# Kernel tuning notes

Measured on AMD Instinct MI355X. Metric: run time of the kernel, lower is better.

The kernel has to match this reference:

```python
import jax, jax.numpy as jnp
import numpy as np

H, DK, DV = 4, 64, 64        # heads, key/value head dims (hidden=256)
M, TOPK = 4, 2               # num memories, router top-k
GN, EPS, COND_SCALE = 16.0, 1e-5, 1.0


def setup_inputs() -> dict:
    key = jax.random.key(0)
    ks = jax.random.split(key, 12)
    B, Q, K, D = 8, 64, 256, 256
    w = lambda k, shape, fan: jax.random.normal(k, shape, jnp.float32) / np.sqrt(fan).astype(np.float32)
    return {
        "query": jax.random.normal(ks[0], (B, Q, D), jnp.float32),
        "keyval": jax.random.normal(ks[1], (B, K, D), jnp.float32),
        "attention_mask_kv": jnp.ones((B, K), jnp.int32),
        "W_cond": w(ks[2], (D, D), D),
        "W_q": w(ks[3], (D, H * DK), D),
        "W_k": w(ks[4], (D, H * DK), D),
        "W_v": w(ks[5], (D, H * DV), D),
        "W_gk1": w(ks[6], (D, 16), D),
        "W_gk2": w(ks[7], (16, H * DK), 16),
        "b_gk2": jnp.zeros((H * DK,), jnp.float32),
        "W_router": w(ks[8], (D, M), D),
        "norm_w": jnp.ones((DV,), jnp.float32),
        "W_o": w(ks[9], (H * DV, D), H * DV),
    }


def _mem_last(q_last, k, v, gk, sel, wgt):
    """Last-token output of one gated linear-attention memory.
    S_t = diag(exp(gk_t)) S_{t-1} + k_t v_t^T ; o_T = q_T S_T.
    q_last: (N,H,DK); k,gk: (N,K,H,DK); v: (N,K,H,DV); sel,wgt: (N,K)."""
    k_e = k * sel[:, :, None, None]
    v_e = v * wgt[:, :, None, None]
    gk_e = gk * sel[:, :, None, None]          # unselected tokens: no decay, no update
    G = jnp.cumsum(gk_e, axis=1)               # (N,K,H,DK), log decays
    decay = jnp.exp(G[:, -1:, :, :] - G)       # remaining decay to last step, <= 1
    s = jnp.einsum('nhd,nthd->nth', q_last, k_e * decay)
    return jnp.einsum('nth,nthv->nhv', s, v_e)


def reference(query, keyval, attention_mask_kv, W_cond, W_q, W_k, W_v,
              W_gk1, W_gk2, b_gk2, W_router, norm_w, W_o):
    B, Q, D = query.shape
    K = keyval.shape[1]
    N = B * Q
    # broadcast KV expansion + cond injection
    cond = (query @ W_cond) * COND_SCALE                         # (B,Q,D)
    x = (keyval[:, None, :, :] + cond[:, :, None, :]).reshape(N, K, D)
    m = jnp.broadcast_to(attention_mask_kv[:, None, :].astype(x.dtype), (B, Q, K)).reshape(N, K)
    # projections
    q = (x @ W_q).reshape(N, K, H, DK)
    k = (x @ W_k).reshape(N, K, H, DK) * m[:, :, None, None]
    v = (x @ W_v).reshape(N, K, H, DV) * m[:, :, None, None]
    gk = (jax.nn.log_sigmoid(x @ W_gk1 @ W_gk2 + b_gk2) / GN).reshape(N, K, H, DK)
    gk = gk * m[:, :, None, None]
    # router: softmax -> top-k -> renormalize
    router_logits = (x @ W_router).reshape(N * K, M)
    probs = jax.nn.softmax(router_logits, axis=-1)
    topv, topi = jax.lax.top_k(probs, TOPK)
    topv = topv / jnp.sum(topv, axis=-1, keepdims=True)
    w_mem = jnp.sum(jax.nn.one_hot(topi, M, dtype=x.dtype) * topv[..., None], axis=-2)
    w_mem = w_mem.reshape(N, K, M)
    # shared memory (always on) + routed memories
    q_last = q[:, -1]
    ones = jnp.ones((N, K), x.dtype)
    o = _mem_last(q_last, k, v, gk, ones, ones)
    for e in range(M):
        we = w_mem[:, :, e]
        o = o + _mem_last(q_last, k, v, gk, (we > 0).astype(x.dtype), we)
    # per-head RMSNorm + output projection
    o = o * jax.lax.rsqrt(jnp.mean(o * o, axis=-1, keepdims=True) + EPS) * norm_w
    out = (o.reshape(N, H * DV) @ W_o).reshape(B, Q, D)
    return out, router_logits
```

## Files before the change

### kernel.cpp

```cpp
#include <hip/hip_runtime.h>
#include <math.h>

#define Hh   4
#define Bb   8
#define Qq   64
#define Kk   256
#define Dd   256
#define Nn   (Bb * Qq)
#define GNf  16.0f
#define EPSf 1e-5f

#define SKV  776
#define SCB  1032

struct GemmS { float As[16][136]; float Ws[16][136]; };
struct RtrS  { float WrT[4][260]; };
union  WorkS { GemmS g; RtrS r; };

__device__ __forceinline__ float wred(float x) {
#pragma unroll
    for (int off = 32; off > 0; off >>= 1)
        x += __shfl_xor(x, off, 64);
    return x;
}

__device__ void gemm64(GemmS& g, const float* __restrict__ A, int lda, int Mv,
                       const float* __restrict__ B, int bn,
                       float* __restrict__ C, int ldc)
{
    float (*As)[68] = (float(*)[68])(&g.As[0][0]);
    const int tid = threadIdx.x;
    const int ty = tid >> 4, tx = tid & 15;
    const int am = tid >> 2, ak = (tid & 3) << 2;
    const int wk = tid >> 4, wc = (tid & 15) << 3;
    const int ams = (am < Mv) ? am : (Mv - 1);

    float acc[4][8] = {};
    const float* aptr = A + (size_t)ams * lda + ak;
    const float* bptr = B + wk * 256 + bn + wc;
    float4 av = *(const float4*)aptr;
    float4 b0 = *(const float4*)bptr;
    float4 b1 = *(const float4*)(bptr + 4);

    for (int k0 = 0; k0 < 256; k0 += 16) {
        __syncthreads();
        As[ak + 0][am] = av.x; As[ak + 1][am] = av.y;
        As[ak + 2][am] = av.z; As[ak + 3][am] = av.w;
        *(float4*)&g.Ws[wk][wc]     = b0;
        *(float4*)&g.Ws[wk][wc + 4] = b1;
        __syncthreads();
        if (k0 + 16 < 256) {
            av = *(const float4*)(aptr + k0 + 16);
            b0 = *(const float4*)(bptr + (k0 + 16) * 256);
            b1 = *(const float4*)(bptr + (k0 + 16) * 256 + 4);
        }
#pragma unroll
        for (int kk = 0; kk < 16; ++kk) {
            const float4 a4 = *(const float4*)&As[kk][ty << 2];
            const float4 w0 = *(const float4*)&g.Ws[kk][tx << 2];
            const float4 w1 = *(const float4*)&g.Ws[kk][64 + (tx << 2)];
            const float a_[4] = {a4.x, a4.y, a4.z, a4.w};
            const float w_[8] = {w0.x, w0.y, w0.z, w0.w, w1.x, w1.y, w1.z, w1.w};
#pragma unroll
            for (int i = 0; i < 4; ++i)
#pragma unroll
                for (int jj = 0; jj < 8; ++jj)
                    acc[i][jj] = fmaf(a_[i], w_[jj], acc[i][jj]);
        }
    }

#pragma unroll
    for (int i = 0; i < 4; ++i) {
        const int rr = (ty << 2) + i;
        if (rr < Mv) {
            *(float4*)(C + (size_t)rr * ldc + (tx << 2)) =
                make_float4(acc[i][0], acc[i][1], acc[i][2], acc[i][3]);
            *(float4*)(C + (size_t)rr * ldc + 64 + (tx << 2)) =
                make_float4(acc[i][4], acc[i][5], acc[i][6], acc[i][7]);
        }
    }
}

__device__ void router_region(RtrS& rs, const float* __restrict__ A,
                              const float* __restrict__ Wr,
                              float* __restrict__ C, int ldc, int row0)
{
    const int tid = threadIdx.x;
    for (int idx = tid; idx < 1024; idx += 256)
        rs.WrT[idx & 3][idx >> 2] = Wr[idx];
    __syncthreads();
    const int row = row0 + (tid >> 2), c = tid & 3;
    const float* a = A + (size_t)row * 256;
    float acc = 0.f;
#pragma unroll 8
    for (int k4 = 0; k4 < 64; ++k4) {
        const float4 avv = *(const float4*)(a + (k4 << 2));
        const float4 wvv = *(const float4*)&rs.WrT[c][k4 << 2];
        acc = fmaf(avv.x, wvv.x, acc);
        acc = fmaf(avv.y, wvv.y, acc);
        acc = fmaf(avv.z, wvv.z, acc);
        acc = fmaf(avv.w, wvv.w, acc);
    }
    C[(size_t)row * ldc + c] = acc;
}

__device__ void wg_region(const float* __restrict__ Wg1,
                          const float* __restrict__ Wg2,
                          float* __restrict__ Wg, int k0)
{
    const int c = threadIdx.x;
    float w2[16];
#pragma unroll
    for (int i = 0; i < 16; ++i) w2[i] = Wg2[i * 256 + c];
#pragma unroll
    for (int r = 0; r < 16; ++r) {
        const int k = k0 + r;
        float s = 0.f;
#pragma unroll
        for (int i = 0; i < 16; ++i) s = fmaf(Wg1[k * 16 + i], w2[i], s);
        Wg[k * 256 + c] = s;
    }
}

__global__ __launch_bounds__(256) void k1(
    const float* __restrict__ query, const float* __restrict__ keyval,
    const float* __restrict__ W_cond, const float* __restrict__ W_q,
    const float* __restrict__ W_gk1, const float* __restrict__ W_gk2,
    const float* __restrict__ W_router,
    float* __restrict__ Wg, float* __restrict__ cond,
    float* __restrict__ qlast, float* __restrict__ KVb)
{
    __shared__ WorkS S;
    const int id = blockIdx.x;
    if (id < 16) {
        wg_region(W_gk1, W_gk2, Wg, id * 16);
    } else if (id < 32) {
        const int t = id - 16;
        gemm64(S.g, query + (size_t)(t >> 1) * 64 * 256, 256, 64,
               W_cond, (t & 1) * 128,
               cond + (size_t)(t >> 1) * 64 * 256 + (t & 1) * 128, 256);
    } else if (id < 34) {
        gemm64(S.g, keyval + 255 * 256, Kk * Dd, 8, W_q, (id - 32) * 128,
               qlast + (id - 32) * 128, 256);
    } else {
        router_region(S.r, keyval, W_router, KVb + 768, SKV, (id - 34) * 64);
    }
}

__global__ __launch_bounds__(256) void k2(
    const float* __restrict__ keyval, const float* __restrict__ cond,
    const float* __restrict__ W_q, const float* __restrict__ W_k,
    const float* __restrict__ W_v, const float* __restrict__ Wg,
    const float* __restrict__ W_router,
    float* __restrict__ KVb, float* __restrict__ Cb)
{
    __shared__ WorkS S;
    const int id = blockIdx.x;
    if (id < 192) {
        const int rt = id / 6, ct = id % 6;
        const float* Bsel = (ct < 2) ? W_k : (ct < 4) ? W_v : Wg;
        gemm64(S.g, keyval + (size_t)rt * 64 * 256, 256, 64,
               Bsel, (ct & 1) * 128,
               KVb + (size_t)rt * 64 * SKV + (ct >> 1) * 256 + (ct & 1) * 128,
               SKV);
    } else if (id < 256) {
        const int t = id - 192, rg = t >> 4, rt = (t & 15) >> 1, ct = t & 1;
        const float* Bsel = (rg == 0) ? W_q : (rg == 1) ? W_k
                          : (rg == 2) ? W_v : Wg;
        gemm64(S.g, cond + (size_t)rt * 64 * 256, 256, 64,
               Bsel, ct * 128,
               Cb + (size_t)rt * 64 * SCB + rg * 256 + ct * 128, SCB);
    } else {
        router_region(S.r, cond, W_router, Cb + 1024, SCB, (id - 256) * 64);
    }
}

__global__ __launch_bounds__(256) void mom_fused(
    const float* __restrict__ KVb, const float* __restrict__ Cb,
    const float* __restrict__ qlast, const float* __restrict__ b_gk2,
    const int* __restrict__ mask, const float* __restrict__ W_o,
    const float* __restrict__ norm_w, float* __restrict__ out,
    float* __restrict__ logits)
{
    __shared__ float4 wm[Kk];
    __shared__ float  Pt[4][16][68];
    __shared__ float  sbuf[4][16];
    __shared__ float  onorm[Dd];

    const int n = blockIdx.x;
    const int b = n >> 6;
    const int j = threadIdx.x;
    const int lane = j & 63;
    const int wv = j >> 6;

    const float qc = Cb[(size_t)n * SCB + j];
    const float kc = Cb[(size_t)n * SCB + 256 + j];
    const float vc = Cb[(size_t)n * SCB + 512 + j];
    const float pc = Cb[(size_t)n * SCB + 768 + j] + b_gk2[j];
    const float4 rc = *(const float4*)(Cb + (size_t)n * SCB + 1024);

    const int* pm = mask + b * Kk;

    {
        const float4 kvr = *(const float4*)(KVb + (size_t)(b * Kk + j) * SKV + 768);
        float l[4] = {kvr.x + rc.x, kvr.y + rc.y, kvr.z + rc.z, kvr.w + rc.w};
        *(float4*)(logits + ((size_t)n * Kk + j) * 4) =
            make_float4(l[0], l[1], l[2], l[3]);

        int i1 = 0;
#pragma unroll
        for (int q = 1; q < 4; ++q) if (l[q] > l[i1]) i1 = q;
        int i2 = -1;
#pragma unroll
        for (int q = 0; q < 4; ++q) {
            if (q == i1) continue;
            if (i2 < 0 || l[q] > l[i2]) i2 = q;
        }
        const float mx = fmaxf(l[i1], l[i2]);
        const float e1 = __expf(l[i1] - mx);
        const float e2 = __expf(l[i2] - mx);
        const float inv = 1.f / (e1 + e2);
        float w[4] = {0.f, 0.f, 0.f, 0.f};
        w[i1] = e1 * inv;
        w[i2] = e2 * inv;
        wm[j] = make_float4(w[0], w[1], w[2], w[3]);
    }
    __syncthreads();

    const float ql  = qlast[b * 256 + j] + qc;
    const float qkc = ql * kc;
    const float* pkv = KVb + (size_t)b * Kk * SKV + j;

    float E0 = 1.f, E1 = 1.f, E2 = 1.f, E3 = 1.f, E4 = 1.f;
    float o = 0.f;
    const int tl = lane & 15, qg = lane >> 4;

    for (int t0 = Kk - 16; t0 >= 0; t0 -= 16) {
        float ka[16], va[16], pa[16];
#pragma unroll
        for (int i = 0; i < 16; ++i) {
            const float* r = pkv + (size_t)(t0 + 15 - i) * SKV;
            ka[i] = r[0];
            va[i] = r[256];
            pa[i] = r[512];
        }
#pragma unroll
        for (int i = 0; i < 16; ++i) {
            const int t = t0 + 15 - i;
            const float mf  = (float)pm[t];
            const float pre = pa[i] + pc;
            const float ee  = __expf(-pre);
            float dg = __expf(-0.0625f * __logf(1.f + ee));
            dg = (mf != 0.f) ? dg : 1.f;
            const float4 w = wm[t];
            const float zf = E0 + w.x * E1 + w.y * E2 + w.z * E3 + w.w * E4;
            const float qlk = fmaf(ql, ka[i], qkc);
            Pt[wv][i][lane] = qlk * zf * mf;
            va[i] = va[i] + vc;
            E0 *= dg;
            E1 *= (w.x > 0.f) ? dg : 1.f;
            E2 *= (w.y > 0.f) ? dg : 1.f;
            E3 *= (w.z > 0.f) ? dg : 1.f;
            E4 *= (w.w > 0.f) ? dg : 1.f;
        }
        __builtin_amdgcn_wave_barrier();

        float s = 0.f;
#pragma unroll
        for (int rr4 = 0; rr4 < 4; ++rr4) {
            const float4 p4 = *(const float4*)&Pt[wv][tl][qg * 16 + rr4 * 4];
            s += (p4.x + p4.y) + (p4.z + p4.w);
        }
        s += __shfl_xor(s, 16, 64);
        s += __shfl_xor(s, 32, 64);
        sbuf[wv][tl] = s;
        __builtin_amdgcn_wave_barrier();
#pragma unroll
        for (int rr4 = 0; rr4 < 4; ++rr4) {
            const float4 sv = *(const float4*)&sbuf[wv][rr4 * 4];
            o = fmaf(sv.x, va[rr4 * 4 + 0], o);
            o = fmaf(sv.y, va[rr4 * 4 + 1], o);
            o = fmaf(sv.z, va[rr4 * 4 + 2], o);
            o = fmaf(sv.w, va[rr4 * 4 + 3], o);
        }
    }

    const float ms = wred(o * o) * (1.0f / 64.0f);
    onorm[j] = o * rsqrtf(ms + EPSf) * norm_w[lane];
    __syncthreads();

    float acc = 0.f;
#pragma unroll 8
    for (int k = 0; k < 256; ++k)
        acc = fmaf(onorm[k], W_o[(size_t)k * 256 + j], acc);
    out[(size_t)n * 256 + j] = acc;
}

extern "C" void kernel_launch(void* const* d_in, const int* in_sizes, int n_in,
                              void* d_out, int out_size, void* d_ws, size_t ws_size,
                              hipStream_t stream)
{
    const float* query    = (const float*)d_in[0];
    const float* keyval   = (const float*)d_in[1];
    const int*   mask     = (const int*)  d_in[2];
    const float* W_cond   = (const float*)d_in[3];
    const float* W_q      = (const float*)d_in[4];
    const float* W_k      = (const float*)d_in[5];
    const float* W_v      = (const float*)d_in[6];
    const float* W_gk1    = (const float*)d_in[7];
    const float* W_gk2    = (const float*)d_in[8];
    const float* b_gk2    = (const float*)d_in[9];
    const float* W_router = (const float*)d_in[10];
    const float* norm_w   = (const float*)d_in[11];
    const float* W_o      = (const float*)d_in[12];

    float* out    = (float*)d_out;
    float* logits = out + Nn * Dd;

    float* p = (float*)d_ws;
    float* Wg    = p; p += 256 * 256;
    float* KVb   = p; p += 2048 * SKV;
    float* cond  = p; p += Nn * 256;
    float* qlast = p; p += 8 * 256;
    float* Cb    = p; p += Nn * SCB;

    k1<<<66, dim3(256), 0, stream>>>(
        query, keyval, W_cond, W_q, W_gk1, W_gk2, W_router,
        Wg, cond, qlast, KVb);

    k2<<<264, dim3(256), 0, stream>>>(
        keyval, cond, W_q, W_k, W_v, Wg, W_router, KVb, Cb);

    mom_fused<<<Nn, dim3(256), 0, stream>>>(
        KVb, Cb, qlast, b_gk2, mask, W_o, norm_w, out, logits);
}
```

Before: 240.5 us.

## Rebalance GEMM kernels into prep/main/cb stages and stream KV loads in scan

Moves the Wg = W_gk1·W_gk2 product into its own small kernel. The keyval GEMMs, cond GEMM, qlast and keyval router now run in one 242-block launch, and a separate 72-block kernel handles the cond-derived GEMMs, so load balance across the launches changes. Row strides SKV/SCB are padded to different sizes, likely to avoid channel or bank conflicts. In the scan kernel, k/v/p loads are issued inline per step instead of batch-prefetched into registers, and log-sigmoid is rewritten in a numerically stable form with the mask folded into the exponent. The extra launch adds overhead, and the inline loads may expose more memory latency.

```diff
diff --git a/kernel.cpp b/kernel.cpp
--- a/kernel.cpp
+++ b/kernel.cpp
@@ -10,8 +10,8 @@
 #define GNf  16.0f
 #define EPSf 1e-5f
 
-#define SKV  776
-#define SCB  1032
+#define SKV  832
+#define SCB  1088
 
 struct GemmS { float As[16][136]; float Ws[16][136]; };
 struct RtrS  { float WrT[4][260]; };
@@ -22,6 +22,19 @@
     for (int off = 32; off > 0; off >>= 1)
         x += __shfl_xor(x, off, 64);
     return x;
+}
+
+__global__ __launch_bounds__(256) void prep(
+    const float* __restrict__ Wg1, const float* __restrict__ Wg2,
+    float* __restrict__ Wg)
+{
+    const int e = blockIdx.x * 256 + threadIdx.x;
+    const int k = e >> 8, c = e & 255;
+    float s = 0.f;
+#pragma unroll
+    for (int i = 0; i < 16; ++i)
+        s = fmaf(Wg1[k * 16 + i], Wg2[i * 256 + c], s);
+    Wg[e] = s;
 }
 
 __device__ void gemm64(GemmS& g, const float* __restrict__ A, int lda, int Mv,
@@ -104,74 +117,61 @@
     C[(size_t)row * ldc + c] = acc;
 }
 
-__device__ void wg_region(const float* __restrict__ Wg1,
-                          const float* __restrict__ Wg2,
-                          float* __restrict__ Wg, int k0)
-{
-    const int c = threadIdx.x;
-    float w2[16];
-#pragma unroll
-    for (int i = 0; i < 16; ++i) w2[i] = Wg2[i * 256 + c];
-#pragma unroll
-    for (int r = 0; r < 16; ++r) {
-        const int k = k0 + r;
-        float s = 0.f;
-#pragma unroll
-        for (int i = 0; i < 16; ++i) s = fmaf(Wg1[k * 16 + i], w2[i], s);
-        Wg[k * 256 + c] = s;
-    }
-}
-
-__global__ __launch_bounds__(256) void k1(
-    const float* __restrict__ query, const float* __restrict__ keyval,
-    const float* __restrict__ W_cond, const float* __restrict__ W_q,
-    const float* __restrict__ W_gk1, const float* __restrict__ W_gk2,
-    const float* __restrict__ W_router,
-    float* __restrict__ Wg, float* __restrict__ cond,
-    float* __restrict__ qlast, float* __restrict__ KVb)
+__global__ __launch_bounds__(256) void gemm_main(
+    const float* __restrict__ keyval, const float* __restrict__ query,
+    const float* __restrict__ W_k, const float* __restrict__ W_v,
+    const float* __restrict__ Wg, const float* __restrict__ W_cond,
+    const float* __restrict__ W_q, const float* __restrict__ W_router,
+    float* __restrict__ KVb, float* __restrict__ cond,
+    float* __restrict__ qlast)
 {
     __shared__ WorkS S;
     const int id = blockIdx.x;
-    if (id < 16) {
-        wg_region(W_gk1, W_gk2, Wg, id * 16);
-    } else if (id < 32) {
-        const int t = id - 16;
-        gemm64(S.g, query + (size_t)(t >> 1) * 64 * 256, 256, 64,
-               W_cond, (t & 1) * 128,
-               cond + (size_t)(t >> 1) * 64 * 256 + (t & 1) * 128, 256);
-    } else if (id < 34) {
-        gemm64(S.g, keyval + 255 * 256, Kk * Dd, 8, W_q, (id - 32) * 128,
-               qlast + (id - 32) * 128, 256);
+    if (id < 210) {
+        const float* A; int lda, Mv; const float* Bm; int bn; float* C; int ldc;
+        if (id < 192) {
+            const int rt = id / 6, ct = id % 6;
+            const float* Bsel; int cbase;
+            if (ct < 2)      { Bsel = W_k; cbase = 0; }
+            else if (ct < 4) { Bsel = W_v; cbase = 256; }
+            else             { Bsel = Wg;  cbase = 512; }
+            A = keyval + (size_t)rt * 64 * 256; lda = 256; Mv = 64;
+            Bm = Bsel; bn = (ct & 1) * 128;
+            C = KVb + (size_t)rt * 64 * SKV + cbase + bn; ldc = SKV;
+        } else if (id < 208) {
+            const int t = id - 192, rt = t >> 1, ct = t & 1;
+            A = query + (size_t)rt * 64 * 256; lda = 256; Mv = 64;
+            Bm = W_cond; bn = ct * 128;
+            C = cond + (size_t)rt * 64 * 256 + ct * 128; ldc = 256;
+        } else {
+            const int ct = id - 208;
+            A = keyval + 255 * 256; lda = Kk * Dd; Mv = 8;
+            Bm = W_q; bn = ct * 128;
+            C = qlast + ct * 128; ldc = 256;
+        }
+        gemm64(S.g, A, lda, Mv, Bm, bn, C, ldc);
     } else {
-        router_region(S.r, keyval, W_router, KVb + 768, SKV, (id - 34) * 64);
-    }
-}
-
-__global__ __launch_bounds__(256) void k2(
-    const float* __restrict__ keyval, const float* __restrict__ cond,
+        router_region(S.r, keyval, W_router, KVb + 768, SKV, (id - 210) * 64);
+    }
+}
+
+__global__ __launch_bounds__(256) void gemm_cb(
+    const float* __restrict__ cond,
     const float* __restrict__ W_q, const float* __restrict__ W_k,
     const float* __restrict__ W_v, const float* __restrict__ Wg,
-    const float* __restrict__ W_router,
-    float* __restrict__ KVb, float* __restrict__ Cb)
+    const float* __restrict__ W_router, float* __restrict__ Cb)
 {
     __shared__ WorkS S;
     const int id = blockIdx.x;
-    if (id < 192) {
-        const int rt = id / 6, ct = id % 6;
-        const float* Bsel = (ct < 2) ? W_k : (ct < 4) ? W_v : Wg;
-        gemm64(S.g, keyval + (size_t)rt * 64 * 256, 256, 64,
-               Bsel, (ct & 1) * 128,
-               KVb + (size_t)rt * 64 * SKV + (ct >> 1) * 256 + (ct & 1) * 128,
-               SKV);
-    } else if (id < 256) {
-        const int t = id - 192, rg = t >> 4, rt = (t & 15) >> 1, ct = t & 1;
+    if (id < 64) {
+        const int rg = id >> 4, t = id & 15, rt = t >> 1, ct = t & 1;
         const float* Bsel = (rg == 0) ? W_q : (rg == 1) ? W_k
                           : (rg == 2) ? W_v : Wg;
         gemm64(S.g, cond + (size_t)rt * 64 * 256, 256, 64,
                Bsel, ct * 128,
                Cb + (size_t)rt * 64 * SCB + rg * 256 + ct * 128, SCB);
     } else {
-        router_region(S.r, cond, W_router, Cb + 1024, SCB, (id - 256) * 64);
+        router_region(S.r, cond, W_router, Cb + 1024, SCB, (id - 64) * 64);
     }
 }
 
@@ -229,34 +229,34 @@
 
     const float ql  = qlast[b * 256 + j] + qc;
     const float qkc = ql * kc;
-    const float* pkv = KVb + (size_t)b * Kk * SKV + j;
+    const float* pk = KVb + (size_t)b * Kk * SKV + j;
+    const float* pv = pk + 256;
+    const float* pp = pk + 512;
 
     float E0 = 1.f, E1 = 1.f, E2 = 1.f, E3 = 1.f, E4 = 1.f;
     float o = 0.f;
     const int tl = lane & 15, qg = lane >> 4;
 
     for (int t0 = Kk - 16; t0 >= 0; t0 -= 16) {
-        float ka[16], va[16], pa[16];
-#pragma unroll
-        for (int i = 0; i < 16; ++i) {
-            const float* r = pkv + (size_t)(t0 + 15 - i) * SKV;
-            ka[i] = r[0];
-            va[i] = r[256];
-            pa[i] = r[512];
-        }
+        float vreg[16];
 #pragma unroll
         for (int i = 0; i < 16; ++i) {
             const int t = t0 + 15 - i;
-            const float mf  = (float)pm[t];
-            const float pre = pa[i] + pc;
-            const float ee  = __expf(-pre);
-            float dg = __expf(-0.0625f * __logf(1.f + ee));
-            dg = (mf != 0.f) ? dg : 1.f;
-            const float4 w = wm[t];
+            const float mf   = (float)pm[t];
+            const float kraw = pk[(size_t)t * SKV];
+            const float vraw = pv[(size_t)t * SKV];
+            const float praw = pp[(size_t)t * SKV];
+            const float pre  = praw + pc;
+
+            const float ls = fminf(pre, 0.f)
+                           - __logf(1.f + __expf(-fabsf(pre)));
+            const float dg = __expf(ls * (0.0625f * mf));
+
+            const float4 w  = wm[t];
             const float zf = E0 + w.x * E1 + w.y * E2 + w.z * E3 + w.w * E4;
-            const float qlk = fmaf(ql, ka[i], qkc);
-            Pt[wv][i][lane] = qlk * zf * mf;
-            va[i] = va[i] + vc;
+            Pt[wv][i][lane] = fmaf(ql, kraw, qkc) * zf * mf;
+            vreg[i] = vraw + vc;
+
             E0 *= dg;
             E1 *= (w.x > 0.f) ? dg : 1.f;
             E2 *= (w.y > 0.f) ? dg : 1.f;
@@ -278,10 +278,10 @@
 #pragma unroll
         for (int rr4 = 0; rr4 < 4; ++rr4) {
             const float4 sv = *(const float4*)&sbuf[wv][rr4 * 4];
-            o = fmaf(sv.x, va[rr4 * 4 + 0], o);
-            o = fmaf(sv.y, va[rr4 * 4 + 1], o);
-            o = fmaf(sv.z, va[rr4 * 4 + 2], o);
-            o = fmaf(sv.w, va[rr4 * 4 + 3], o);
+            o = fmaf(sv.x, vreg[rr4 * 4 + 0], o);
+            o = fmaf(sv.y, vreg[rr4 * 4 + 1], o);
+            o = fmaf(sv.z, vreg[rr4 * 4 + 2], o);
+            o = fmaf(sv.w, vreg[rr4 * 4 + 3], o);
         }
     }
 
@@ -324,12 +324,12 @@
     float* qlast = p; p += 8 * 256;
     float* Cb    = p; p += Nn * SCB;
 
-    k1<<<66, dim3(256), 0, stream>>>(
-        query, keyval, W_cond, W_q, W_gk1, W_gk2, W_router,
-        Wg, cond, qlast, KVb);
-
-    k2<<<264, dim3(256), 0, stream>>>(
-        keyval, cond, W_q, W_k, W_v, Wg, W_router, KVb, Cb);
+    prep<<<256, dim3(256), 0, stream>>>(W_gk1, W_gk2, Wg);
+
+    gemm_main<<<242, dim3(256), 0, stream>>>(
+        keyval, query, W_k, W_v, Wg, W_cond, W_q, W_router, KVb, cond, qlast);
+
+    gemm_cb<<<72, dim3(256), 0, stream>>>(cond, W_q, W_k, W_v, Wg, W_router, Cb);
 
     mom_fused<<<Nn, dim3(256), 0, stream>>>(
         KVb, Cb, qlast, b_gk2, mask, W_o, norm_w, out, logits);
```

After: 221.3 us. -8.0%, faster.
